# Kernel optimization log

Hardware: AMD Instinct MI355X
Metric: run time of the kernel (lower is better)

## Reference

```python
import jax, jax.numpy as jnp
import numpy as np

N_NODES = 50000
N_EDGES = 600000
N_GRAPHS = 64
D_FEAT = 128
DIM_H = 128
N_HOPS = 3
OUT_DIM = 10


def setup_inputs() -> dict:
    key = jax.random.key(0)
    ks = jax.random.split(key, 16)
    x = jax.random.normal(ks[0], (N_NODES, D_FEAT), dtype=jnp.float32)
    edge_index = jax.random.randint(ks[1], (2, N_EDGES), 0, N_NODES, dtype=jnp.int64)
    batch = jnp.sort(jax.random.randint(ks[2], (N_NODES,), 0, N_GRAPHS, dtype=jnp.int64))
    def glorot(k, shape):
        fan = shape[0] + shape[1]
        return jax.random.uniform(k, shape, jnp.float32, -1.0, 1.0) * np.sqrt(6.0 / fan)
    # GCNConv weights stored as [in, out]; Linear weights stored as [in, out]
    W1 = glorot(ks[3], (D_FEAT, DIM_H)); b1 = jnp.zeros((DIM_H,), jnp.float32)
    W2 = glorot(ks[4], (DIM_H, DIM_H)); b2 = jnp.zeros((DIM_H,), jnp.float32)
    W3 = glorot(ks[5], (DIM_H, DIM_H)); b3 = jnp.zeros((DIM_H,), jnp.float32)
    H3 = DIM_H * N_HOPS
    lin1_W = glorot(ks[6], (H3, H3)); lin1_b = jnp.zeros((H3,), jnp.float32)
    lin2_W = glorot(ks[7], (H3, OUT_DIM)); lin2_b = jnp.zeros((OUT_DIM,), jnp.float32)
    return {"x": x, "W1": W1, "b1": b1, "W2": W2, "b2": b2, "W3": W3, "b3": b3,
            "lin1_W": lin1_W, "lin1_b": lin1_b, "lin2_W": lin2_W, "lin2_b": lin2_b,
            "edge_index": edge_index, "batch": batch}


def gcn_conv(x, W, b, src, dst, n_nodes):
    # PyG GCNConv (add_self_loops=True, normalize=True):
    #   deg[i] = in-degree at target + 1 (self loop); norm = d^-1/2[src] * d^-1/2[dst]
    deg = jnp.zeros((n_nodes,), x.dtype).at[dst].add(1.0) + 1.0
    dinv = jax.lax.rsqrt(deg)
    xw = x @ W  # [N, H] transform before propagate
    coef = (dinv[src] * dinv[dst])[:, None]
    agg = jnp.zeros_like(xw).at[dst].add(xw[src] * coef)
    agg = agg + xw * (dinv * dinv)[:, None]  # self-loop messages
    return agg + b


def global_mean_pool(h, batch, n_graphs):
    sums = jax.ops.segment_sum(h, batch, num_segments=n_graphs)
    cnt = jax.ops.segment_sum(jnp.ones((h.shape[0],), h.dtype), batch, num_segments=n_graphs)
    return sums / jnp.maximum(cnt, 1.0)[:, None]


def reference(x, W1, b1, W2, b2, W3, b3, lin1_W, lin1_b, lin2_W, lin2_b, edge_index, batch):
    src, dst = edge_index[0], edge_index[1]
    n = x.shape[0]
    h1 = gcn_conv(x, W1, b1, src, dst, n)
    h2 = gcn_conv(h1, W2, b2, src, dst, n)
    h3 = gcn_conv(h2, W3, b3, src, dst, n)
    pooled = jnp.concatenate([global_mean_pool(h, batch, N_GRAPHS) for h in (h1, h2, h3)], axis=1)
    h = jax.nn.relu(pooled @ lin1_W + lin1_b)
    # dropout is identity in eval mode
    h = h @ lin2_W + lin2_b
    return (h, jax.nn.log_softmax(h, axis=1))
```

## Files before the change

### kernel.cpp

```cpp
#include <hip/hip_runtime.h>
#include <hip/hip_fp16.h>
#include <math.h>

#define N_NODES 50000
#define N_EDGES 600000
#define N_GRAPHS 64
#define DFEAT 128
#define H3 384
#define OUTD 10
#define SCAN_BLOCKS 196
#define POOL_CHUNKS 16
#define APAD 136

typedef _Float16 f16x8 __attribute__((ext_vector_type(8)));
typedef float f32x4 __attribute__((ext_vector_type(4)));
typedef float f32x2 __attribute__((ext_vector_type(2)));

__global__ __launch_bounds__(256) void k_deg(const int* __restrict__ ei, int* __restrict__ deg,
                                             int* __restrict__ rank) {
    int e = blockIdx.x * 256 + threadIdx.x;
    if (e >= N_EDGES) return;
    int dst = ei[N_EDGES + e];
    rank[e] = atomicAdd(&deg[dst], 1);
}

__global__ __launch_bounds__(256) void k_part(const int* __restrict__ deg, int* __restrict__ part) {
    __shared__ int red[256];
    int tid = threadIdx.x;
    int i = blockIdx.x * 256 + tid;
    red[tid] = (i < N_NODES) ? deg[i] : 0;
    __syncthreads();
    for (int s = 128; s > 0; s >>= 1) {
        if (tid < s) red[tid] += red[tid + s];
        __syncthreads();
    }
    if (tid == 0) part[blockIdx.x] = red[0];
}

__global__ __launch_bounds__(256) void k_scanpart(const int* __restrict__ part, int* __restrict__ base) {
    __shared__ int buf[256];
    int tid = threadIdx.x;
    int v = (tid < SCAN_BLOCKS) ? part[tid] : 0;
    buf[tid] = v;
    __syncthreads();
    for (int d = 1; d < 256; d <<= 1) {
        int t = (tid >= d) ? buf[tid - d] : 0;
        __syncthreads();
        buf[tid] += t;
        __syncthreads();
    }
    if (tid < SCAN_BLOCKS) base[tid] = buf[tid] - v;
}

__global__ __launch_bounds__(256) void k_offsets(const int* __restrict__ deg, const int* __restrict__ base,
                                                 int* __restrict__ offs, float* __restrict__ dinv) {
    __shared__ int buf[256];
    int tid = threadIdx.x;
    int i = blockIdx.x * 256 + tid;
    int v = (i < N_NODES) ? deg[i] : 0;
    buf[tid] = v;
    __syncthreads();
    for (int d = 1; d < 256; d <<= 1) {
        int t = (tid >= d) ? buf[tid - d] : 0;
        __syncthreads();
        buf[tid] += t;
        __syncthreads();
    }
    if (i < N_NODES) {
        int excl = base[blockIdx.x] + buf[tid] - v;
        offs[i] = excl;
        dinv[i] = rsqrtf((float)v + 1.0f);
        if (i == N_NODES - 1) offs[N_NODES] = base[blockIdx.x] + buf[tid];
    }
}

__global__ __launch_bounds__(256) void k_fill(const int* __restrict__ ei, const int* __restrict__ offs,
                                              const int* __restrict__ rank, const float* __restrict__ dinv,
                                              unsigned int* __restrict__ epack) {
    int e = blockIdx.x * 256 + threadIdx.x;
    if (e >= N_EDGES) return;
    int s = ei[e];
    int t = ei[N_EDGES + e];
    unsigned short dh = __half_as_ushort(__float2half(dinv[s]));
    epack[offs[t] + rank[e]] = (unsigned int)s | ((unsigned int)dh << 16);
}

__global__ __launch_bounds__(256) void k_prep(const float* __restrict__ W1, const float* __restrict__ W2,
                                              const float* __restrict__ W3, _Float16* __restrict__ Wt,
                                              float* __restrict__ pooled) {
    int b = blockIdx.x;
    if (b < 192) {
        int idx = b * 256 + threadIdx.x;
        int l = idx >> 14, r = idx & 16383;
        const float* W = (l == 0) ? W1 : (l == 1) ? W2 : W3;
        int k = r >> 7, n = r & 127;
        Wt[l * 16384 + n * 128 + k] = (_Float16)W[k * 128 + n];
    } else {
        int idx = (b - 192) * 256 + threadIdx.x;
        if (idx < N_GRAPHS * H3) pooled[idx] = 0.0f;
    }
}

template <bool A_FP16>
__global__ __launch_bounds__(256) void gemm_mfma(const void* __restrict__ Aptr, const _Float16* __restrict__ Wt,
                                                 unsigned char* __restrict__ T, int M) {
    __shared__ _Float16 As[64 * APAD];
    __shared__ _Float16 Ws[128 * APAD];
    int tid = threadIdx.x;
    int base = blockIdx.x * 64;
    for (int c = tid; c < 2048; c += 256) {
        int n = c >> 4, c8 = (c & 15) << 3;
        *(f16x8*)&Ws[n * APAD + c8] = *(const f16x8*)&Wt[n * 128 + c8];
    }
    for (int c = tid; c < 1024; c += 256) {
        int r = c >> 4, c8 = (c & 15) << 3;
        int gr = base + r; if (gr >= M) gr = M - 1;
        if (A_FP16) {
            const _Float16* A = (const _Float16*)Aptr;
            *(f16x8*)&As[r * APAD + c8] = *(const f16x8*)&A[(size_t)gr * 128 + c8];
        } else {
            const float* A = (const float*)Aptr;
            const float* src = A + (size_t)gr * 128 + c8;
            float4 v0 = *(const float4*)(src);
            float4 v1 = *(const float4*)(src + 4);
            f16x8 h;
            h[0] = (_Float16)v0.x; h[1] = (_Float16)v0.y; h[2] = (_Float16)v0.z; h[3] = (_Float16)v0.w;
            h[4] = (_Float16)v1.x; h[5] = (_Float16)v1.y; h[6] = (_Float16)v1.z; h[7] = (_Float16)v1.w;
            *(f16x8*)&As[r * APAD + c8] = h;
        }
    }
    __syncthreads();
    int wave = tid >> 6, lane = tid & 63;
    int m = lane & 15, quad = lane >> 4;
    f32x4 acc[8];
#pragma unroll
    for (int ct = 0; ct < 8; ++ct) acc[ct] = (f32x4){0.f, 0.f, 0.f, 0.f};
#pragma unroll
    for (int kc = 0; kc < 4; ++kc) {
        f16x8 a = *(const f16x8*)&As[(wave * 16 + m) * APAD + kc * 32 + quad * 8];
#pragma unroll
        for (int ct = 0; ct < 8; ++ct) {
            f16x8 b = *(const f16x8*)&Ws[(ct * 16 + m) * APAD + kc * 32 + quad * 8];
            acc[ct] = __builtin_amdgcn_mfma_f32_16x16x32_f16(b, a, acc[ct], 0, 0, 0);
        }
    }
    int node = base + wave * 16 + m;
    if (node < M) {
#pragma unroll
        for (int ct = 0; ct < 8; ++ct) {
            int col = ct * 16 + quad * 4;
            int p = __builtin_amdgcn_cvt_pk_fp8_f32(acc[ct][0], acc[ct][1], 0, false);
            p     = __builtin_amdgcn_cvt_pk_fp8_f32(acc[ct][2], acc[ct][3], p, true);
            *(int*)(T + (size_t)node * 128 + col) = p;
        }
    }
}

__global__ __launch_bounds__(256) void gather_agg(const unsigned int* __restrict__ T32,
                                                  const unsigned int* __restrict__ epack,
                                                  const int* __restrict__ offs,
                                                  const float* __restrict__ dinv, const float* __restrict__ bias,
                                                  __half2* __restrict__ H2) {
    int h = threadIdx.x >> 5;
    int l32 = threadIdx.x & 31;
    int node = blockIdx.x * 8 + h;
    float di = dinv[node];
    float a0 = 0.f, a1 = 0.f, a2 = 0.f, a3 = 0.f;
    int lo = offs[node], hi = offs[node + 1];
    int e = lo;
    for (; e + 8 <= hi; e += 8) {
        unsigned p0 = epack[e + 0], p1 = epack[e + 1], p2 = epack[e + 2], p3 = epack[e + 3];
        unsigned p4 = epack[e + 4], p5 = epack[e + 5], p6 = epack[e + 6], p7 = epack[e + 7];
        unsigned u0 = T32[(size_t)(p0 & 0xffff) * 32 + l32];
        unsigned u1 = T32[(size_t)(p1 & 0xffff) * 32 + l32];
        unsigned u2 = T32[(size_t)(p2 & 0xffff) * 32 + l32];
        unsigned u3 = T32[(size_t)(p3 & 0xffff) * 32 + l32];
        unsigned u4 = T32[(size_t)(p4 & 0xffff) * 32 + l32];
        unsigned u5 = T32[(size_t)(p5 & 0xffff) * 32 + l32];
        unsigned u6 = T32[(size_t)(p6 & 0xffff) * 32 + l32];
        unsigned u7 = T32[(size_t)(p7 & 0xffff) * 32 + l32];
        float c0 = __half2float(__ushort_as_half((unsigned short)(p0 >> 16)));
        float c1 = __half2float(__ushort_as_half((unsigned short)(p1 >> 16)));
        float c2 = __half2float(__ushort_as_half((unsigned short)(p2 >> 16)));
        float c3 = __half2float(__ushort_as_half((unsigned short)(p3 >> 16)));
        float c4 = __half2float(__ushort_as_half((unsigned short)(p4 >> 16)));
        float c5 = __half2float(__ushort_as_half((unsigned short)(p5 >> 16)));
        float c6 = __half2float(__ushort_as_half((unsigned short)(p6 >> 16)));
        float c7 = __half2float(__ushort_as_half((unsigned short)(p7 >> 16)));
        f32x2 lo0 = __builtin_amdgcn_cvt_pk_f32_fp8(u0, false), hi0 = __builtin_amdgcn_cvt_pk_f32_fp8(u0, true);
        f32x2 lo1 = __builtin_amdgcn_cvt_pk_f32_fp8(u1, false), hi1 = __builtin_amdgcn_cvt_pk_f32_fp8(u1, true);
        f32x2 lo2 = __builtin_amdgcn_cvt_pk_f32_fp8(u2, false), hi2 = __builtin_amdgcn_cvt_pk_f32_fp8(u2, true);
        f32x2 lo3 = __builtin_amdgcn_cvt_pk_f32_fp8(u3, false), hi3 = __builtin_amdgcn_cvt_pk_f32_fp8(u3, true);
        f32x2 lo4 = __builtin_amdgcn_cvt_pk_f32_fp8(u4, false), hi4 = __builtin_amdgcn_cvt_pk_f32_fp8(u4, true);
        f32x2 lo5 = __builtin_amdgcn_cvt_pk_f32_fp8(u5, false), hi5 = __builtin_amdgcn_cvt_pk_f32_fp8(u5, true);
        f32x2 lo6 = __builtin_amdgcn_cvt_pk_f32_fp8(u6, false), hi6 = __builtin_amdgcn_cvt_pk_f32_fp8(u6, true);
        f32x2 lo7 = __builtin_amdgcn_cvt_pk_f32_fp8(u7, false), hi7 = __builtin_amdgcn_cvt_pk_f32_fp8(u7, true);
        a0 += lo0.x * c0; a1 += lo0.y * c0; a2 += hi0.x * c0; a3 += hi0.y * c0;
        a0 += lo1.x * c1; a1 += lo1.y * c1; a2 += hi1.x * c1; a3 += hi1.y * c1;
        a0 += lo2.x * c2; a1 += lo2.y * c2; a2 += hi2.x * c2; a3 += hi2.y * c2;
        a0 += lo3.x * c3; a1 += lo3.y * c3; a2 += hi3.x * c3; a3 += hi3.y * c3;
        a0 += lo4.x * c4; a1 += lo4.y * c4; a2 += hi4.x * c4; a3 += hi4.y * c4;
        a0 += lo5.x * c5; a1 += lo5.y * c5; a2 += hi5.x * c5; a3 += hi5.y * c5;
        a0 += lo6.x * c6; a1 += lo6.y * c6; a2 += hi6.x * c6; a3 += hi6.y * c6;
        a0 += lo7.x * c7; a1 += lo7.y * c7; a2 += hi7.x * c7; a3 += hi7.y * c7;
    }
    for (; e + 4 <= hi; e += 4) {
        unsigned p0 = epack[e + 0], p1 = epack[e + 1], p2 = epack[e + 2], p3 = epack[e + 3];
        unsigned u0 = T32[(size_t)(p0 & 0xffff) * 32 + l32];
        unsigned u1 = T32[(size_t)(p1 & 0xffff) * 32 + l32];
        unsigned u2 = T32[(size_t)(p2 & 0xffff) * 32 + l32];
        unsigned u3 = T32[(size_t)(p3 & 0xffff) * 32 + l32];
        float c0 = __half2float(__ushort_as_half((unsigned short)(p0 >> 16)));
        float c1 = __half2float(__ushort_as_half((unsigned short)(p1 >> 16)));
        float c2 = __half2float(__ushort_as_half((unsigned short)(p2 >> 16)));
        float c3 = __half2float(__ushort_as_half((unsigned short)(p3 >> 16)));
        f32x2 lo0 = __builtin_amdgcn_cvt_pk_f32_fp8(u0, false), hi0 = __builtin_amdgcn_cvt_pk_f32_fp8(u0, true);
        f32x2 lo1 = __builtin_amdgcn_cvt_pk_f32_fp8(u1, false), hi1 = __builtin_amdgcn_cvt_pk_f32_fp8(u1, true);
        f32x2 lo2 = __builtin_amdgcn_cvt_pk_f32_fp8(u2, false), hi2 = __builtin_amdgcn_cvt_pk_f32_fp8(u2, true);
        f32x2 lo3 = __builtin_amdgcn_cvt_pk_f32_fp8(u3, false), hi3 = __builtin_amdgcn_cvt_pk_f32_fp8(u3, true);
        a0 += lo0.x * c0; a1 += lo0.y * c0; a2 += hi0.x * c0; a3 += hi0.y * c0;
        a0 += lo1.x * c1; a1 += lo1.y * c1; a2 += hi1.x * c1; a3 += hi1.y * c1;
        a0 += lo2.x * c2; a1 += lo2.y * c2; a2 += hi2.x * c2; a3 += hi2.y * c2;
        a0 += lo3.x * c3; a1 += lo3.y * c3; a2 += hi3.x * c3; a3 += hi3.y * c3;
    }
    for (; e < hi; ++e) {
        unsigned p = epack[e];
        float c = __half2float(__ushort_as_half((unsigned short)(p >> 16)));
        unsigned u = T32[(size_t)(p & 0xffff) * 32 + l32];
        f32x2 tl = __builtin_amdgcn_cvt_pk_f32_fp8(u, false), th = __builtin_amdgcn_cvt_pk_f32_fp8(u, true);
        a0 += tl.x * c; a1 += tl.y * c; a2 += th.x * c; a3 += th.y * c;
    }
    unsigned su = T32[(size_t)node * 32 + l32];
    f32x2 sl = __builtin_amdgcn_cvt_pk_f32_fp8(su, false), sh = __builtin_amdgcn_cvt_pk_f32_fp8(su, true);
    float4 b4 = *(const float4*)(bias + l32 * 4);
    float dd = di * di;
    float r0 = di * a0 + sl.x * dd + b4.x;
    float r1 = di * a1 + sl.y * dd + b4.y;
    float r2 = di * a2 + sh.x * dd + b4.z;
    float r3 = di * a3 + sh.y * dd + b4.w;
    H2[(size_t)node * 64 + l32 * 2]     = __floats2half2_rn(r0, r1);
    H2[(size_t)node * 64 + l32 * 2 + 1] = __floats2half2_rn(r2, r3);
}

__global__ __launch_bounds__(256) void pool_kernel(const __half2* __restrict__ H0,
                                                   const __half2* __restrict__ H1,
                                                   const __half2* __restrict__ H2buf,
                                                   const int* __restrict__ batch,
                                                   float* __restrict__ pooled) {
    __shared__ int bounds[2];
    __shared__ float2 red[256];
    int g = blockIdx.x >> 4;
    int chunk = blockIdx.x & (POOL_CHUNKS - 1);
    int tid = threadIdx.x;
    int d2 = tid & 63, sub = tid >> 6;
    if (tid < 2) {
        int target = g + tid;
        int lo = 0, hi = N_NODES;
        while (lo < hi) {
            int mid = (lo + hi) >> 1;
            if (batch[mid] < target) lo = mid + 1; else hi = mid;
        }
        bounds[tid] = lo;
    }
    __syncthreads();
    int lo = bounds[0], hi = bounds[1];
    int n = hi - lo;
    int per = (n + POOL_CHUNKS - 1) / POOL_CHUNKS;
    int s = lo + chunk * per;
    int e = s + per; if (e > hi) e = hi;
    const __half2* Hs[3] = {H0, H1, H2buf};
    for (int l = 0; l < 3; ++l) {
        const __half2* H = Hs[l];
        float ax = 0.0f, ay = 0.0f;
        for (int r = s + sub; r < e; r += 4) {
            float2 v = __half22float2(H[(size_t)r * 64 + d2]);
            ax += v.x; ay += v.y;
        }
        red[tid] = make_float2(ax, ay);
        __syncthreads();
        if (sub == 0 && s < e) {
            float2 v0 = red[d2], v1 = red[64 + d2], v2 = red[128 + d2], v3 = red[192 + d2];
            atomicAdd(&pooled[g * H3 + l * 128 + d2 * 2],     v0.x + v1.x + v2.x + v3.x);
            atomicAdd(&pooled[g * H3 + l * 128 + d2 * 2 + 1], v0.y + v1.y + v2.y + v3.y);
        }
        __syncthreads();
    }
}

__global__ __launch_bounds__(384) void mlp_kernel(const float* __restrict__ pooled,
                                                  const int* __restrict__ batch,
                                                  const float* __restrict__ l1W, const float* __restrict__ l1b,
                                                  const float* __restrict__ l2W, const float* __restrict__ l2b,
                                                  float* __restrict__ out) {
    __shared__ float p[H3];
    __shared__ float hid[H3];
    __shared__ float o10[OUTD];
    __shared__ int bnd[2];
    int g = blockIdx.x, tid = threadIdx.x;
    if (tid < 2) {
        int target = g + tid;
        int lo = 0, hi = N_NODES;
        while (lo < hi) {
            int mid = (lo + hi) >> 1;
            if (batch[mid] < target) lo = mid + 1; else hi = mid;
        }
        bnd[tid] = lo;
    }
    __syncthreads();
    float inv = 1.0f / fmaxf((float)(bnd[1] - bnd[0]), 1.0f);
    p[tid] = pooled[g * H3 + tid] * inv;
    __syncthreads();
    float acc = l1b[tid];
    for (int k = 0; k < H3; ++k) acc += p[k] * l1W[k * H3 + tid];
    hid[tid] = fmaxf(acc, 0.0f);
    __syncthreads();
    if (tid < OUTD) {
        float o = l2b[tid];
        for (int k = 0; k < H3; ++k) o += hid[k] * l2W[k * OUTD + tid];
        o10[tid] = o;
        out[g * OUTD + tid] = o;
    }
    __syncthreads();
    if (tid == 0) {
        float m = o10[0];
        for (int j = 1; j < OUTD; ++j) m = fmaxf(m, o10[j]);
        float s = 0.0f;
        for (int j = 0; j < OUTD; ++j) s += expf(o10[j] - m);
        float lse = m + logf(s);
        for (int j = 0; j < OUTD; ++j) out[N_GRAPHS * OUTD + g * OUTD + j] = o10[j] - lse;
    }
}

extern "C" void kernel_launch(void* const* d_in, const int* in_sizes, int n_in,
                              void* d_out, int out_size, void* d_ws, size_t ws_size,
                              hipStream_t stream) {
    const float* x      = (const float*)d_in[0];
    const float* W1     = (const float*)d_in[1];
    const float* b1     = (const float*)d_in[2];
    const float* W2     = (const float*)d_in[3];
    const float* b2     = (const float*)d_in[4];
    const float* W3     = (const float*)d_in[5];
    const float* b3     = (const float*)d_in[6];
    const float* lin1_W = (const float*)d_in[7];
    const float* lin1_b = (const float*)d_in[8];
    const float* lin2_W = (const float*)d_in[9];
    const float* lin2_b = (const float*)d_in[10];
    const int* edge_index = (const int*)d_in[11];
    const int* batch      = (const int*)d_in[12];

    char* ws = (char*)d_ws;
    auto alloc = [&](size_t bytes) -> void* {
        void* p = (void*)ws;
        ws += (bytes + 255) & ~(size_t)255;
        return p;
    };
    int*   deg    = (int*)  alloc((size_t)N_NODES * 4);
    int*   part   = (int*)  alloc((size_t)SCAN_BLOCKS * 4);
    int*   pbase  = (int*)  alloc((size_t)SCAN_BLOCKS * 4);
    int*   offs   = (int*)  alloc((size_t)(N_NODES + 1) * 4);
    int*   rank   = (int*)  alloc((size_t)N_EDGES * 4);
    float* dinv   = (float*)alloc((size_t)N_NODES * 4);
    unsigned int* epack = (unsigned int*)alloc((size_t)N_EDGES * 4);
    unsigned char* T = (unsigned char*)alloc((size_t)N_NODES * 128);
    __half* Hbuf[3];
    for (int l = 0; l < 3; ++l) Hbuf[l] = (__half*)alloc((size_t)N_NODES * 128 * 2);
    _Float16* Wt  = (_Float16*)alloc((size_t)3 * 128 * 128 * 2);
    float* pooled = (float*)alloc((size_t)N_GRAPHS * H3 * 4);

    hipMemsetAsync(deg, 0, (size_t)N_NODES * 4, stream);
    k_deg<<<(N_EDGES + 255) / 256, 256, 0, stream>>>(edge_index, deg, rank);
    k_part<<<SCAN_BLOCKS, 256, 0, stream>>>(deg, part);
    k_scanpart<<<1, 256, 0, stream>>>(part, pbase);
    k_offsets<<<SCAN_BLOCKS, 256, 0, stream>>>(deg, pbase, offs, dinv);
    k_fill<<<(N_EDGES + 255) / 256, 256, 0, stream>>>(edge_index, offs, rank, dinv, epack);
    k_prep<<<288, 256, 0, stream>>>(W1, W2, W3, Wt, pooled);

    const float* bs[3] = {b1, b2, b3};
    for (int l = 0; l < 3; ++l) {
        if (l == 0)
            gemm_mfma<false><<<(N_NODES + 63) / 64, 256, 0, stream>>>(x, Wt, T, N_NODES);
        else
            gemm_mfma<true><<<(N_NODES + 63) / 64, 256, 0, stream>>>(Hbuf[l - 1], Wt + (size_t)l * 16384, T, N_NODES);
        gather_agg<<<N_NODES / 8, 256, 0, stream>>>((const unsigned int*)T, epack, offs, dinv, bs[l], (__half2*)Hbuf[l]);
    }
    pool_kernel<<<N_GRAPHS * POOL_CHUNKS, 256, 0, stream>>>((const __half2*)Hbuf[0], (const __half2*)Hbuf[1],
                                                            (const __half2*)Hbuf[2], batch, pooled);
    mlp_kernel<<<N_GRAPHS, 384, 0, stream>>>(pooled, batch, lin1_W, lin1_b, lin2_W, lin2_b, (float*)d_out);
}
```

Measured before the change: 283.3 us.

## Fuse mean-pool into gather kernel via atomics and merge fill/prep launches

Drops the separate pool kernel. Each gather_agg thread now atomically adds its four output values into the pooled buffer of its node's graph. It also merges the edge-fill kernel and the weight-transpose/zero-init kernel into one launch. The goal is to skip re-reading the three fp16 hidden buffers and to save kernel launches. The cost is millions of float atomics per layer aimed at only 64×128 addresses per layer, so contention is heavy, and the summation order becomes nondeterministic.

```diff
diff --git a/kernel.cpp b/kernel.cpp
--- a/kernel.cpp
+++ b/kernel.cpp
@@ -9,7 +9,7 @@
 #define H3 384
 #define OUTD 10
 #define SCAN_BLOCKS 196
-#define POOL_CHUNKS 16
+#define FILL_BLOCKS 2344
 #define APAD 136
 
 typedef _Float16 f16x8 __attribute__((ext_vector_type(8)));
@@ -74,29 +74,28 @@
     }
 }
 
-__global__ __launch_bounds__(256) void k_fill(const int* __restrict__ ei, const int* __restrict__ offs,
-                                              const int* __restrict__ rank, const float* __restrict__ dinv,
-                                              unsigned int* __restrict__ epack) {
-    int e = blockIdx.x * 256 + threadIdx.x;
-    if (e >= N_EDGES) return;
-    int s = ei[e];
-    int t = ei[N_EDGES + e];
-    unsigned short dh = __half_as_ushort(__float2half(dinv[s]));
-    epack[offs[t] + rank[e]] = (unsigned int)s | ((unsigned int)dh << 16);
-}
-
-__global__ __launch_bounds__(256) void k_prep(const float* __restrict__ W1, const float* __restrict__ W2,
-                                              const float* __restrict__ W3, _Float16* __restrict__ Wt,
-                                              float* __restrict__ pooled) {
+__global__ __launch_bounds__(256) void k_fill_prep(const int* __restrict__ ei, const int* __restrict__ offs,
+                                                   const int* __restrict__ rank, const float* __restrict__ dinv,
+                                                   unsigned int* __restrict__ epack,
+                                                   const float* __restrict__ W1, const float* __restrict__ W2,
+                                                   const float* __restrict__ W3, _Float16* __restrict__ Wt,
+                                                   float* __restrict__ pooled) {
     int b = blockIdx.x;
-    if (b < 192) {
-        int idx = b * 256 + threadIdx.x;
+    if (b < FILL_BLOCKS) {
+        int e = b * 256 + threadIdx.x;
+        if (e >= N_EDGES) return;
+        int s = ei[e];
+        int t = ei[N_EDGES + e];
+        unsigned short dh = __half_as_ushort(__float2half(dinv[s]));
+        epack[offs[t] + rank[e]] = (unsigned int)s | ((unsigned int)dh << 16);
+    } else if (b < FILL_BLOCKS + 192) {
+        int idx = (b - FILL_BLOCKS) * 256 + threadIdx.x;
         int l = idx >> 14, r = idx & 16383;
         const float* W = (l == 0) ? W1 : (l == 1) ? W2 : W3;
         int k = r >> 7, n = r & 127;
         Wt[l * 16384 + n * 128 + k] = (_Float16)W[k * 128 + n];
     } else {
-        int idx = (b - 192) * 256 + threadIdx.x;
+        int idx = (b - FILL_BLOCKS - 192) * 256 + threadIdx.x;
         if (idx < N_GRAPHS * H3) pooled[idx] = 0.0f;
     }
 }
@@ -160,6 +159,8 @@
                                                   const unsigned int* __restrict__ epack,
                                                   const int* __restrict__ offs,
                                                   const float* __restrict__ dinv, const float* __restrict__ bias,
+                                                  const int* __restrict__ batch,
+                                                  float* __restrict__ pooledL,
                                                   __half2* __restrict__ H2) {
     int h = threadIdx.x >> 5;
     int l32 = threadIdx.x & 31;
@@ -240,51 +241,12 @@
     float r3 = di * a3 + sh.y * dd + b4.w;
     H2[(size_t)node * 64 + l32 * 2]     = __floats2half2_rn(r0, r1);
     H2[(size_t)node * 64 + l32 * 2 + 1] = __floats2half2_rn(r2, r3);
-}
-
-__global__ __launch_bounds__(256) void pool_kernel(const __half2* __restrict__ H0,
-                                                   const __half2* __restrict__ H1,
-                                                   const __half2* __restrict__ H2buf,
-                                                   const int* __restrict__ batch,
-                                                   float* __restrict__ pooled) {
-    __shared__ int bounds[2];
-    __shared__ float2 red[256];
-    int g = blockIdx.x >> 4;
-    int chunk = blockIdx.x & (POOL_CHUNKS - 1);
-    int tid = threadIdx.x;
-    int d2 = tid & 63, sub = tid >> 6;
-    if (tid < 2) {
-        int target = g + tid;
-        int lo = 0, hi = N_NODES;
-        while (lo < hi) {
-            int mid = (lo + hi) >> 1;
-            if (batch[mid] < target) lo = mid + 1; else hi = mid;
-        }
-        bounds[tid] = lo;
-    }
-    __syncthreads();
-    int lo = bounds[0], hi = bounds[1];
-    int n = hi - lo;
-    int per = (n + POOL_CHUNKS - 1) / POOL_CHUNKS;
-    int s = lo + chunk * per;
-    int e = s + per; if (e > hi) e = hi;
-    const __half2* Hs[3] = {H0, H1, H2buf};
-    for (int l = 0; l < 3; ++l) {
-        const __half2* H = Hs[l];
-        float ax = 0.0f, ay = 0.0f;
-        for (int r = s + sub; r < e; r += 4) {
-            float2 v = __half22float2(H[(size_t)r * 64 + d2]);
-            ax += v.x; ay += v.y;
-        }
-        red[tid] = make_float2(ax, ay);
-        __syncthreads();
-        if (sub == 0 && s < e) {
-            float2 v0 = red[d2], v1 = red[64 + d2], v2 = red[128 + d2], v3 = red[192 + d2];
-            atomicAdd(&pooled[g * H3 + l * 128 + d2 * 2],     v0.x + v1.x + v2.x + v3.x);
-            atomicAdd(&pooled[g * H3 + l * 128 + d2 * 2 + 1], v0.y + v1.y + v2.y + v3.y);
-        }
-        __syncthreads();
-    }
+    int g = batch[node];
+    float* pg = pooledL + (size_t)g * H3 + l32 * 4;
+    atomicAdd(pg + 0, r0);
+    atomicAdd(pg + 1, r1);
+    atomicAdd(pg + 2, r2);
+    atomicAdd(pg + 3, r3);
 }
 
 __global__ __launch_bounds__(384) void mlp_kernel(const float* __restrict__ pooled,
@@ -372,8 +334,8 @@
     k_part<<<SCAN_BLOCKS, 256, 0, stream>>>(deg, part);
     k_scanpart<<<1, 256, 0, stream>>>(part, pbase);
     k_offsets<<<SCAN_BLOCKS, 256, 0, stream>>>(deg, pbase, offs, dinv);
-    k_fill<<<(N_EDGES + 255) / 256, 256, 0, stream>>>(edge_index, offs, rank, dinv, epack);
-    k_prep<<<288, 256, 0, stream>>>(W1, W2, W3, Wt, pooled);
+    k_fill_prep<<<FILL_BLOCKS + 192 + 96, 256, 0, stream>>>(edge_index, offs, rank, dinv, epack,
+                                                            W1, W2, W3, Wt, pooled);
 
     const float* bs[3] = {b1, b2, b3};
     for (int l = 0; l < 3; ++l) {
@@ -381,9 +343,8 @@
             gemm_mfma<false><<<(N_NODES + 63) / 64, 256, 0, stream>>>(x, Wt, T, N_NODES);
         else
             gemm_mfma<true><<<(N_NODES + 63) / 64, 256, 0, stream>>>(Hbuf[l - 1], Wt + (size_t)l * 16384, T, N_NODES);
-        gather_agg<<<N_NODES / 8, 256, 0, stream>>>((const unsigned int*)T, epack, offs, dinv, bs[l], (__half2*)Hbuf[l]);
-    }
-    pool_kernel<<<N_GRAPHS * POOL_CHUNKS, 256, 0, stream>>>((const __half2*)Hbuf[0], (const __half2*)Hbuf[1],
-                                                            (const __half2*)Hbuf[2], batch, pooled);
+        gather_agg<<<N_NODES / 8, 256, 0, stream>>>((const unsigned int*)T, epack, offs, dinv, bs[l],
+                                                    batch, pooled + l * 128, (__half2*)Hbuf[l]);
+    }
     mlp_kernel<<<N_GRAPHS, 384, 0, stream>>>(pooled, batch, lin1_W, lin1_b, lin2_W, lin2_b, (float*)d_out);
 }
```

New measurement: 1.022 ms. 3.61x slower.
